# Performance work log

Measured on AMD Instinct MI355X. Metric: run time of the kernel, lower is better.

Reference implementation:

```python
import jax, jax.numpy as jnp
import numpy as np

NH = 8  # num_heads
EPS_LN = 1e-5
BN_DENOM = float(np.sqrt(1.0 + 1e-5))  # eval-mode BN with running_mean=0, running_var=1


def _layernorm(x, g, b):
    m = jnp.mean(x, axis=-1, keepdims=True)
    v = jnp.var(x, axis=-1, keepdims=True)
    return (x - m) * jax.lax.rsqrt(v + EPS_LN) * g + b


def _rope(q, k):
    # q,k: [B, H, T, D]
    t, d = q.shape[2], q.shape[3]
    half = d // 2
    pos = jnp.arange(t, dtype=q.dtype)[:, None]
    idx = jnp.arange(half, dtype=q.dtype)[None, :]
    inv_freq = 1.0 / (10000.0 ** (idx / half))
    ang = pos * inv_freq  # [T, half]
    sin = jnp.sin(ang)[None, None]
    cos = jnp.cos(ang)[None, None]

    def rot(x):
        x1, x2 = x[..., :half], x[..., half:]
        return jnp.concatenate([x1 * cos - x2 * sin, x1 * sin + x2 * cos], axis=-1)

    return rot(q), rot(k)


def _sep_conv(y, dw, pw):
    # y: [B, C, T]; dw: [C, 1, K]; pw: [O, C]
    c = y.shape[1]
    k = dw.shape[-1]
    y = jax.lax.conv_general_dilated(
        y, dw, window_strides=(2,), padding=[(k // 2, k // 2)],
        dimension_numbers=('NCH', 'OIH', 'NCH'), feature_group_count=c)
    return jnp.einsum('bct,oc->bot', y, pw)


def _attn(h, Wq, bq, Wk, bk, Wv, bv, Wo, bo):
    b, t, e = h.shape
    hd = e // NH
    scale = hd ** -0.5

    def split(z):
        return jnp.transpose(z.reshape(b, t, NH, hd), (0, 2, 1, 3))

    q = split(h @ Wq.T + bq)
    k = split(h @ Wk.T + bk)
    v = split(h @ Wv.T + bv)
    q, k = _rope(q, k)
    logits = jnp.einsum('bhtd,bhsd->bhts', q, k) * scale
    attn = jax.nn.softmax(logits, axis=-1)
    ctx = jnp.einsum('bhts,bhsd->bhtd', attn, v)
    ctx = jnp.transpose(ctx, (0, 2, 1, 3)).reshape(b, t, e)
    return ctx @ Wo.T + bo


def setup_inputs() -> dict:
    key = jax.random.key(0)
    ks = jax.random.split(key, 40)
    B, T, Cin = 8, 4096, 64
    E, L, MLP = 256, 6, 1024
    s = 0.02
    p = {}
    p['x'] = jax.random.normal(ks[0], (B, T, Cin), jnp.float32)
    p['conv1_dw'] = jax.random.normal(ks[1], (Cin, 1, 7), jnp.float32) * s
    p['conv1_pw'] = jax.random.normal(ks[2], (64, Cin), jnp.float32) * s
    p['bn1_g'] = jnp.ones((64,), jnp.float32)
    p['bn1_b'] = jnp.zeros((64,), jnp.float32)
    p['conv2_dw'] = jax.random.normal(ks[3], (64, 1, 7), jnp.float32) * s
    p['conv2_pw'] = jax.random.normal(ks[4], (128, 64), jnp.float32) * s
    p['bn2_g'] = jnp.ones((128,), jnp.float32)
    p['bn2_b'] = jnp.zeros((128,), jnp.float32)
    p['proj_w'] = jax.random.normal(ks[5], (E, 128), jnp.float32) * s
    p['proj_b'] = jnp.zeros((E,), jnp.float32)
    p['cls_tok'] = jax.random.normal(ks[6], (1, 1, E), jnp.float32) * s
    p['Wq'] = jax.random.normal(ks[7], (L, E, E), jnp.float32) * s
    p['bq'] = jnp.zeros((L, E), jnp.float32)
    p['Wk'] = jax.random.normal(ks[8], (L, E, E), jnp.float32) * s
    p['bk'] = jnp.zeros((L, E), jnp.float32)
    p['Wv'] = jax.random.normal(ks[9], (L, E, E), jnp.float32) * s
    p['bv'] = jnp.zeros((L, E), jnp.float32)
    p['Wo'] = jax.random.normal(ks[10], (L, E, E), jnp.float32) * s
    p['bo'] = jnp.zeros((L, E), jnp.float32)
    p['ln1_g'] = jnp.ones((L, E), jnp.float32)
    p['ln1_b'] = jnp.zeros((L, E), jnp.float32)
    p['mlp_w1'] = jax.random.normal(ks[11], (L, MLP, E), jnp.float32) * s
    p['mlp_b1'] = jnp.zeros((L, MLP), jnp.float32)
    p['mlp_w2'] = jax.random.normal(ks[12], (L, E, MLP), jnp.float32) * s
    p['mlp_b2'] = jnp.zeros((L, E), jnp.float32)
    p['ln2_g'] = jnp.ones((L, E), jnp.float32)
    p['ln2_b'] = jnp.zeros((L, E), jnp.float32)
    p['lat_w'] = jax.random.normal(ks[13], (E, E), jnp.float32) * s
    p['lat_b'] = jnp.zeros((E,), jnp.float32)
    p['latn_g'] = jnp.ones((E,), jnp.float32)
    p['latn_b'] = jnp.zeros((E,), jnp.float32)
    p['ts_w'] = jax.random.normal(ks[14], (1, E), jnp.float32) * s
    p['ts_b'] = jnp.zeros((1,), jnp.float32)
    return p


def reference(x, conv1_dw, conv1_pw, bn1_g, bn1_b, conv2_dw, conv2_pw, bn2_g, bn2_b,
              proj_w, proj_b, cls_tok, Wq, bq, Wk, bk, Wv, bv, Wo, bo,
              ln1_g, ln1_b, mlp_w1, mlp_b1, mlp_w2, mlp_b2, ln2_g, ln2_b,
              lat_w, lat_b, latn_g, latn_b, ts_w, ts_b):
    B = x.shape[0]
    y = jnp.transpose(x, (0, 2, 1))  # [B, C, T]
    y = _sep_conv(y, conv1_dw, conv1_pw)
    y = (y / BN_DENOM) * bn1_g[None, :, None] + bn1_b[None, :, None]
    y = jax.nn.gelu(y, approximate=False)
    y = _sep_conv(y, conv2_dw, conv2_pw)
    y = (y / BN_DENOM) * bn2_g[None, :, None] + bn2_b[None, :, None]
    y = jax.nn.gelu(y, approximate=False)
    y = jnp.transpose(y, (0, 2, 1))  # [B, T', 128]
    h = y @ proj_w.T + proj_b  # [B, T', E]
    h = jnp.concatenate([jnp.broadcast_to(cls_tok, (B, 1, h.shape[-1])), h], axis=1)
    L = Wq.shape[0]
    for i in range(L):
        a = _attn(h, Wq[i], bq[i], Wk[i], bk[i], Wv[i], bv[i], Wo[i], bo[i])
        h = _layernorm(h + a, ln1_g[i], ln1_b[i])
        m = jax.nn.gelu(h @ mlp_w1[i].T + mlp_b1[i], approximate=False) @ mlp_w2[i].T + mlp_b2[i]
        h = _layernorm(h + m, ln2_g[i], ln2_b[i])
    h = _layernorm(h @ lat_w.T + lat_b, latn_g, latn_b)
    logits = h[:, 1:] @ ts_w.T + ts_b  # per-time-step logits (CLS excluded)
    return logits
```

## Files before the change

### kernel.cpp

```cpp
#include <hip/hip_runtime.h>
#include <hip/hip_bf16.h>
#include <math.h>

typedef __hip_bfloat16 bf16;
typedef __attribute__((ext_vector_type(8))) short bf16x8_t;
typedef __attribute__((ext_vector_type(4))) short bf16x4_t;
typedef __attribute__((ext_vector_type(4))) float f32x4_t;

#define BN_RDENOM 0.9999950000374997f
#define EPS_LN 1e-5f
#define ATTN_SCALE 0.17677669529663687f
#define S_LEN 1025
#define S_PAD 1088
#define E_DIM 256
#define NHEAD 8
#define HDIM 32
#define MROWS (8 * S_LEN)
#define WSLOT 786432

__device__ __forceinline__ float bf(const bf16 v) { return __bfloat162float(v); }
__device__ __forceinline__ bf16 tobf(float v) { return __float2bfloat16(v); }
__device__ __forceinline__ short bfbits(float v) {
    bf16 t = __float2bfloat16(v); short s; __builtin_memcpy(&s, &t, 2); return s;
}
__device__ __forceinline__ float gelu_exact(float x) {
    return 0.5f * x * (1.0f + erff(x * 0.70710678118654752f));
}

#define DPP_ROR(x, N) __int_as_float(__builtin_amdgcn_update_dpp(0, __float_as_int(x), 0x120 + (N), 0xF, 0xF, false))
__device__ __forceinline__ float row_allsum(float x) {
    x = x + DPP_ROR(x, 1);
    x = x + DPP_ROR(x, 2);
    x = x + DPP_ROR(x, 4);
    x = x + DPP_ROR(x, 8);
    return x;
}

__global__ __launch_bounds__(256) void cvt_w(const float* __restrict__ src,
    bf16* __restrict__ dst, int n)
{
    int i = (blockIdx.x * 256 + threadIdx.x) * 4;
    if (i >= n) return;
    f32x4_t v = *(const f32x4_t*)(src + i);
    bf16x4_t o;
    #pragma unroll
    for (int j = 0; j < 4; ++j) o[j] = bfbits(v[j]);
    *(bf16x4_t*)((short*)dst + i) = o;
}

__global__ __launch_bounds__(256) void cvt_layer6(const float* __restrict__ wq,
    const float* __restrict__ wk, const float* __restrict__ wv, const float* __restrict__ wo,
    const float* __restrict__ w1, const float* __restrict__ w2, bf16* __restrict__ dst)
{
    int l = blockIdx.y;
    int i = (blockIdx.x * 256 + threadIdx.x) * 4;
    const float* s; int off;
    if (i < 262144) {
        s = (i < 65536) ? wq : (i < 131072) ? wk : (i < 196608) ? wv : wo;
        s += (size_t)l * 65536;
        off = i & 65535;
    } else if (i < 524288) { s = w1 + (size_t)l * 262144; off = i - 262144; }
    else                   { s = w2 + (size_t)l * 262144; off = i - 524288; }
    f32x4_t v = *(const f32x4_t*)(s + off);
    bf16x4_t o;
    #pragma unroll
    for (int j = 0; j < 4; ++j) o[j] = bfbits(v[j]);
    *(bf16x4_t*)((short*)dst + (size_t)l * WSLOT + i) = o;
}

__global__ __launch_bounds__(256) void conv_sep1(const float* __restrict__ x,
    const float* __restrict__ dw, const float* __restrict__ pw,
    const float* __restrict__ g, const float* __restrict__ bb,
    bf16* __restrict__ out)
{
    __shared__ float xs[70][64];
    __shared__ float dy[32][64];
    __shared__ float pws[64][65];
    __shared__ float dws[64][7];
    int blk = blockIdx.x;
    int tile = blk & 63, b = blk >> 6;
    int t0 = tile * 32;
    int tid = threadIdx.x;
    int tbase = t0 * 2 - 3;
    for (int i = tid; i < 70 * 64; i += 256) {
        int r = i >> 6, c = i & 63;
        int t = tbase + r;
        xs[r][c] = (t >= 0 && t < 4096) ? x[((size_t)b * 4096 + t) * 64 + c] : 0.f;
    }
    for (int i = tid; i < 64 * 7; i += 256) dws[i / 7][i % 7] = dw[i];
    for (int i = tid; i < 64 * 64; i += 256) pws[i >> 6][i & 63] = pw[i];
    __syncthreads();
    for (int i = tid; i < 32 * 64; i += 256) {
        int tl = i >> 6, c = i & 63;
        float s = 0.f;
        #pragma unroll
        for (int j = 0; j < 7; ++j) s += xs[2 * tl + j][c] * dws[c][j];
        dy[tl][c] = s;
    }
    __syncthreads();
    for (int i = tid; i < 32 * 64; i += 256) {
        int tl = i >> 6, o = i & 63;
        float s = 0.f;
        #pragma unroll 8
        for (int c = 0; c < 64; ++c) s += dy[tl][c] * pws[o][c];
        s = s * BN_RDENOM * g[o] + bb[o];
        out[((size_t)(b * 2048 + t0 + tl)) * 64 + o] = tobf(gelu_exact(s));
    }
}

__global__ __launch_bounds__(256) void conv_sep2(const bf16* __restrict__ x,
    const float* __restrict__ dw, const float* __restrict__ pw,
    const float* __restrict__ g, const float* __restrict__ bb,
    bf16* __restrict__ out)
{
    __shared__ float xs[70][64];
    __shared__ float dy[32][64];
    __shared__ float pws[128][65];
    __shared__ float dws[64][7];
    int blk = blockIdx.x;
    int tile = blk & 31, b = blk >> 5;
    int t0 = tile * 32;
    int tid = threadIdx.x;
    int tbase = t0 * 2 - 3;
    for (int i = tid; i < 70 * 64; i += 256) {
        int r = i >> 6, c = i & 63;
        int t = tbase + r;
        xs[r][c] = (t >= 0 && t < 2048) ? bf(x[((size_t)b * 2048 + t) * 64 + c]) : 0.f;
    }
    for (int i = tid; i < 64 * 7; i += 256) dws[i / 7][i % 7] = dw[i];
    for (int i = tid; i < 128 * 64; i += 256) pws[i >> 6][i & 63] = pw[i];
    __syncthreads();
    for (int i = tid; i < 32 * 64; i += 256) {
        int tl = i >> 6, c = i & 63;
        float s = 0.f;
        #pragma unroll
        for (int j = 0; j < 7; ++j) s += xs[2 * tl + j][c] * dws[c][j];
        dy[tl][c] = s;
    }
    __syncthreads();
    for (int i = tid; i < 32 * 128; i += 256) {
        int tl = i >> 7, o = i & 127;
        float s = 0.f;
        #pragma unroll 8
        for (int c = 0; c < 64; ++c) s += dy[tl][c] * pws[o][c];
        s = s * BN_RDENOM * g[o] + bb[o];
        out[((size_t)(b * 1024 + t0 + tl)) * 128 + o] = tobf(gelu_exact(s));
    }
}

template <int ACT>
__global__ __launch_bounds__(256) void gemm_bf(const bf16* __restrict__ A,
    const bf16* __restrict__ W, const float* __restrict__ bias,
    bf16* __restrict__ C, int M, int N, int K)
{
    __shared__ short As[64 * 72];
    __shared__ short Bs[64 * 72];
    int tid = threadIdx.x;
    int wave = tid >> 6, lane = tid & 63, quad = lane >> 4, l16 = lane & 15;
    int wm = wave & 1, wn = wave >> 1;
    int m0 = blockIdx.x * 64, n0 = blockIdx.y * 64;

    f32x4_t zero4 = {0.f, 0.f, 0.f, 0.f};
    f32x4_t acc[2][2];
    acc[0][0] = zero4; acc[0][1] = zero4; acc[1][0] = zero4; acc[1][1] = zero4;

    int srow = tid >> 2, skc = (tid & 3) * 16;
    for (int k0 = 0; k0 < K; k0 += 64) {
        {
            int m = m0 + srow;
            bf16x8_t a0 = {}, a1 = {};
            if (m < M) {
                a0 = *(const bf16x8_t*)(A + (size_t)m * K + k0 + skc);
                a1 = *(const bf16x8_t*)(A + (size_t)m * K + k0 + skc + 8);
            }
            *(bf16x8_t*)(&As[srow * 72 + skc])     = a0;
            *(bf16x8_t*)(&As[srow * 72 + skc + 8]) = a1;
        }
        {
            const bf16* wp = W + (size_t)(n0 + srow) * K + k0 + skc;
            *(bf16x8_t*)(&Bs[srow * 72 + skc])     = *(const bf16x8_t*)(wp);
            *(bf16x8_t*)(&Bs[srow * 72 + skc + 8]) = *(const bf16x8_t*)(wp + 8);
        }
        __syncthreads();
        #pragma unroll
        for (int ks = 0; ks < 2; ++ks) {
            bf16x8_t a[2], b[2];
            #pragma unroll
            for (int mi = 0; mi < 2; ++mi)
                a[mi] = *(bf16x8_t*)(&As[(wm * 32 + mi * 16 + l16) * 72 + ks * 32 + quad * 8]);
            #pragma unroll
            for (int ni = 0; ni < 2; ++ni)
                b[ni] = *(bf16x8_t*)(&Bs[(wn * 32 + ni * 16 + l16) * 72 + ks * 32 + quad * 8]);
            #pragma unroll
            for (int mi = 0; mi < 2; ++mi)
                #pragma unroll
                for (int ni = 0; ni < 2; ++ni)
                    acc[mi][ni] = __builtin_amdgcn_mfma_f32_16x16x32_bf16(a[mi], b[ni], acc[mi][ni], 0, 0, 0);
        }
        __syncthreads();
    }
    #pragma unroll
    for (int mi = 0; mi < 2; ++mi) {
        #pragma unroll
        for (int ni = 0; ni < 2; ++ni) {
            int col = n0 + wn * 32 + ni * 16 + l16;
            float bv = bias[col];
            #pragma unroll
            for (int r = 0; r < 4; ++r) {
                int row = m0 + wm * 32 + mi * 16 + quad * 4 + r;
                if (row < M) {
                    float v = acc[mi][ni][r] + bv;
                    if (ACT == 1) v = gelu_exact(v);
                    C[(size_t)row * N + col] = tobf(v);
                }
            }
        }
    }
}

template <int ACT>
__global__ __launch_bounds__(256) void gemm_bf128(const bf16* __restrict__ A,
    const bf16* __restrict__ W, const float* __restrict__ bias,
    bf16* __restrict__ C, int M, int N, int K)
{
    __shared__ short As[128 * 72];
    __shared__ short Bs[64 * 72];
    int tid = threadIdx.x;
    int wave = tid >> 6, lane = tid & 63, quad = lane >> 4, l16 = lane & 15;
    int wm = wave & 1, wn = wave >> 1;
    int m0 = blockIdx.x * 128, n0 = blockIdx.y * 64;

    f32x4_t zero4 = {0.f, 0.f, 0.f, 0.f};
    f32x4_t acc[4][2];
    #pragma unroll
    for (int i = 0; i < 4; ++i) { acc[i][0] = zero4; acc[i][1] = zero4; }

    int srow = tid >> 2, skc = (tid & 3) * 16;
    for (int k0 = 0; k0 < K; k0 += 64) {
        #pragma unroll
        for (int p = 0; p < 2; ++p) {
            int row = srow + p * 64;
            int m = m0 + row;
            bf16x8_t a0 = {}, a1 = {};
            if (m < M) {
                a0 = *(const bf16x8_t*)(A + (size_t)m * K + k0 + skc);
                a1 = *(const bf16x8_t*)(A + (size_t)m * K + k0 + skc + 8);
            }
            *(bf16x8_t*)(&As[row * 72 + skc])     = a0;
            *(bf16x8_t*)(&As[row * 72 + skc + 8]) = a1;
        }
        {
            const bf16* wp = W + (size_t)(n0 + srow) * K + k0 + skc;
            *(bf16x8_t*)(&Bs[srow * 72 + skc])     = *(const bf16x8_t*)(wp);
            *(bf16x8_t*)(&Bs[srow * 72 + skc + 8]) = *(const bf16x8_t*)(wp + 8);
        }
        __syncthreads();
        #pragma unroll
        for (int ks = 0; ks < 2; ++ks) {
            bf16x8_t a[4], b[2];
            #pragma unroll
            for (int mi = 0; mi < 4; ++mi)
                a[mi] = *(bf16x8_t*)(&As[(wm * 64 + mi * 16 + l16) * 72 + ks * 32 + quad * 8]);
            #pragma unroll
            for (int ni = 0; ni < 2; ++ni)
                b[ni] = *(bf16x8_t*)(&Bs[(wn * 32 + ni * 16 + l16) * 72 + ks * 32 + quad * 8]);
            #pragma unroll
            for (int mi = 0; mi < 4; ++mi)
                #pragma unroll
                for (int ni = 0; ni < 2; ++ni)
                    acc[mi][ni] = __builtin_amdgcn_mfma_f32_16x16x32_bf16(a[mi], b[ni], acc[mi][ni], 0, 0, 0);
        }
        __syncthreads();
    }
    #pragma unroll
    for (int mi = 0; mi < 4; ++mi) {
        #pragma unroll
        for (int ni = 0; ni < 2; ++ni) {
            int col = n0 + wn * 32 + ni * 16 + l16;
            float bv = bias[col];
            #pragma unroll
            for (int r = 0; r < 4; ++r) {
                int row = m0 + wm * 64 + mi * 16 + quad * 4 + r;
                if (row < M) {
                    float v = acc[mi][ni][r] + bv;
                    if (ACT == 1) v = gelu_exact(v);
                    C[(size_t)row * N + col] = tobf(v);
                }
            }
        }
    }
}

__global__ __launch_bounds__(256) void gemm_qkv128(const bf16* __restrict__ A,
    const bf16* __restrict__ Wqkv, const float* __restrict__ bq,
    const float* __restrict__ bk, const float* __restrict__ bv,
    bf16* __restrict__ qo, bf16* __restrict__ ko, bf16* __restrict__ vo, int M)
{
    const int K = 256, N = 256;
    __shared__ short As[128 * 72];
    __shared__ short Bs[64 * 72];
    int part = blockIdx.y >> 2;
    int n0 = (blockIdx.y & 3) * 64;
    const bf16* W     = Wqkv + (size_t)part * 65536;
    const float* bias = (part == 0) ? bq : (part == 1) ? bk : bv;
    bf16* C           = (part == 0) ? qo : (part == 1) ? ko : vo;
    bool dorope = (part < 2);
    float oscale = (part == 0) ? ATTN_SCALE : 1.0f;

    int tid = threadIdx.x;
    int wave = tid >> 6, lane = tid & 63, quad = lane >> 4, l16 = lane & 15;
    int wm = wave & 1, wn = wave >> 1;
    int m0 = blockIdx.x * 128;

    f32x4_t zero4 = {0.f, 0.f, 0.f, 0.f};
    f32x4_t acc[4][2];
    #pragma unroll
    for (int i = 0; i < 4; ++i) { acc[i][0] = zero4; acc[i][1] = zero4; }

    int srow = tid >> 2, skc = (tid & 3) * 16;
    for (int k0 = 0; k0 < K; k0 += 64) {
        #pragma unroll
        for (int p = 0; p < 2; ++p) {
            int row = srow + p * 64;
            int m = m0 + row;
            bf16x8_t a0 = {}, a1 = {};
            if (m < M) {
                a0 = *(const bf16x8_t*)(A + (size_t)m * K + k0 + skc);
                a1 = *(const bf16x8_t*)(A + (size_t)m * K + k0 + skc + 8);
            }
            *(bf16x8_t*)(&As[row * 72 + skc])     = a0;
            *(bf16x8_t*)(&As[row * 72 + skc + 8]) = a1;
        }
        {
            const bf16* wp = W + (size_t)(n0 + srow) * K + k0 + skc;
            *(bf16x8_t*)(&Bs[srow * 72 + skc])     = *(const bf16x8_t*)(wp);
            *(bf16x8_t*)(&Bs[srow * 72 + skc + 8]) = *(const bf16x8_t*)(wp + 8);
        }
        __syncthreads();
        #pragma unroll
        for (int ks = 0; ks < 2; ++ks) {
            bf16x8_t a[4], b[2];
            #pragma unroll
            for (int mi = 0; mi < 4; ++mi)
                a[mi] = *(bf16x8_t*)(&As[(wm * 64 + mi * 16 + l16) * 72 + ks * 32 + quad * 8]);
            #pragma unroll
            for (int ni = 0; ni < 2; ++ni)
                b[ni] = *(bf16x8_t*)(&Bs[(wn * 32 + ni * 16 + l16) * 72 + ks * 32 + quad * 8]);
            #pragma unroll
            for (int mi = 0; mi < 4; ++mi)
                #pragma unroll
                for (int ni = 0; ni < 2; ++ni)
                    acc[mi][ni] = __builtin_amdgcn_mfma_f32_16x16x32_bf16(a[mi], b[ni], acc[mi][ni], 0, 0, 0);
        }
        __syncthreads();
    }
    int col0 = n0 + wn * 32 + l16;
    float b1v = bias[col0], b2v = bias[col0 + 16];
    float invf = powf(10000.f, -(float)l16 * (1.f / 16.f));
    #pragma unroll
    for (int mi = 0; mi < 4; ++mi) {
        #pragma unroll
        for (int r = 0; r < 4; ++r) {
            int row = m0 + wm * 64 + mi * 16 + quad * 4 + r;
            if (row >= M) continue;
            int bb = row / S_LEN, t = row - bb * S_LEN;
            float x1 = acc[mi][0][r] + b1v;
            float x2 = acc[mi][1][r] + b2v;
            if (dorope) {
                float ang = (float)t * invf;
                float sn, cs;
                __sincosf(ang, &sn, &cs);
                float y1 = (x1 * cs - x2 * sn) * oscale;
                float y2 = (x1 * sn + x2 * cs) * oscale;
                x1 = y1; x2 = y2;
            }
            size_t obase = ((size_t)bb * S_PAD + t) * N;
            C[obase + col0]      = tobf(x1);
            C[obase + col0 + 16] = tobf(x2);
        }
    }
}

__global__ __launch_bounds__(256) void assemble_h(const bf16* __restrict__ tmp,
    const float* __restrict__ cls, bf16* __restrict__ h)
{
    int row = blockIdx.x;
    int tid = threadIdx.x;
    int b = row / S_LEN, t = row % S_LEN;
    bf16 v = (t == 0) ? tobf(cls[tid]) : tmp[((size_t)(b * 1024 + t - 1)) * E_DIM + tid];
    h[(size_t)row * E_DIM + tid] = v;
}

__global__ __launch_bounds__(256) void attn_mfma(const bf16* __restrict__ Q,
    const bf16* __restrict__ K, const bf16* __restrict__ V, bf16* __restrict__ O)
{
    __shared__ short VTs[2][32 * 72];
    __shared__ short Ps[4][16 * 72];
    int blk = blockIdx.x;
    int bh = blk & 63;
    int qt = blk >> 6;
    int hh = bh & 7, b = bh >> 3;
    int tid = threadIdx.x;
    int wave = tid >> 6, lane = tid & 63, quad = lane >> 4, l16 = lane & 15;
    int q0 = qt * 64 + wave * 16;
    const size_t bSp = (size_t)b * S_PAD;
    const size_t bS  = (size_t)b * S_LEN;
    const size_t hoff = (size_t)hh * HDIM;
    const bf16* Qb = Q + bSp * E_DIM + hoff;
    const bf16* Kb = K + bSp * E_DIM + hoff;
    const bf16* Vb = V + bSp * E_DIM + hoff;

    f32x4_t zero4 = {0.f, 0.f, 0.f, 0.f};
    bf16x8_t qfrag = *(const bf16x8_t*)(Qb + (size_t)(q0 + l16) * E_DIM + quad * 8);
    f32x4_t o0 = zero4, o1 = zero4;
    float lsum[4] = {0.f, 0.f, 0.f, 0.f};

    int vs = tid >> 2, vd = (tid & 3) * 8;
    short* myP = Ps[wave];

    bf16x8_t vpre = *(const bf16x8_t*)(Vb + (size_t)vs * E_DIM + vd);

    for (int c = 0; c < 17; ++c) {
        int s0 = c * 64;
        short* VT = VTs[c & 1];
        #pragma unroll
        for (int j = 0; j < 8; ++j) VT[(vd + j) * 72 + vs] = vpre[j];
        if (c < 16)
            vpre = *(const bf16x8_t*)(Vb + (size_t)(s0 + 64 + vs) * E_DIM + vd);
        f32x4_t sc[4];
        #pragma unroll
        for (int kk = 0; kk < 4; ++kk) {
            bf16x8_t kf = *(const bf16x8_t*)(Kb + (size_t)(s0 + kk * 16 + l16) * E_DIM + quad * 8);
            sc[kk] = __builtin_amdgcn_mfma_f32_16x16x32_bf16(qfrag, kf, zero4, 0, 0, 0);
        }
        #pragma unroll
        for (int r = 0; r < 4; ++r) {
            float ps = 0.f;
            #pragma unroll
            for (int kk = 0; kk < 4; ++kk) {
                int s = s0 + kk * 16 + l16;
                float raw = (s < S_LEN) ? sc[kk][r] : -1e30f;
                float p = __expf(raw);
                ps += p;
                myP[(quad * 4 + r) * 72 + kk * 16 + l16] = bfbits(p);
            }
            lsum[r] += ps;
        }
        __syncthreads();
        #pragma unroll
        for (int half = 0; half < 2; ++half) {
            int off = half * 32 + quad * 8;
            bf16x8_t pf  = *(bf16x8_t*)(&myP[l16 * 72 + off]);
            bf16x8_t vf0 = *(bf16x8_t*)(&VT[l16 * 72 + off]);
            bf16x8_t vf1 = *(bf16x8_t*)(&VT[(16 + l16) * 72 + off]);
            o0 = __builtin_amdgcn_mfma_f32_16x16x32_bf16(pf, vf0, o0, 0, 0, 0);
            o1 = __builtin_amdgcn_mfma_f32_16x16x32_bf16(pf, vf1, o1, 0, 0, 0);
        }
    }
    #pragma unroll
    for (int r = 0; r < 4; ++r) {
        int qrow = q0 + quad * 4 + r;
        if (qrow < S_LEN) {
            float rs = 1.f / row_allsum(lsum[r]);
            O[(bS + qrow) * E_DIM + hoff + l16]      = tobf(o0[r] * rs);
            O[(bS + qrow) * E_DIM + hoff + 16 + l16] = tobf(o1[r] * rs);
        }
    }
}

__global__ __launch_bounds__(256) void ln_kernel(const bf16* __restrict__ X,
    const bf16* __restrict__ R, const float* __restrict__ g,
    const float* __restrict__ b, bf16* __restrict__ out)
{
    int wave = threadIdx.x >> 6, lane = threadIdx.x & 63;
    int row0 = blockIdx.x * 8 + wave * 2;
    size_t base0 = (size_t)row0 * E_DIM + lane * 4;
    size_t base1 = base0 + E_DIM;
    float v0[4], v1[4];
    {
        bf16x4_t xa = *(const bf16x4_t*)(X + base0);
        bf16x4_t xb = *(const bf16x4_t*)(X + base1);
        #pragma unroll
        for (int i = 0; i < 4; ++i) {
            bf16 t; short s;
            s = xa[i]; __builtin_memcpy(&t, &s, 2); v0[i] = bf(t);
            s = xb[i]; __builtin_memcpy(&t, &s, 2); v1[i] = bf(t);
        }
    }
    if (R) {
        bf16x4_t ra = *(const bf16x4_t*)(R + base0);
        bf16x4_t rb = *(const bf16x4_t*)(R + base1);
        #pragma unroll
        for (int i = 0; i < 4; ++i) {
            bf16 t; short s;
            s = ra[i]; __builtin_memcpy(&t, &s, 2); v0[i] += bf(t);
            s = rb[i]; __builtin_memcpy(&t, &s, 2); v1[i] += bf(t);
        }
    }
    float s0 = v0[0] + v0[1] + v0[2] + v0[3];
    float s1 = v1[0] + v1[1] + v1[2] + v1[3];
    #pragma unroll
    for (int off = 32; off; off >>= 1) { s0 += __shfl_xor(s0, off); s1 += __shfl_xor(s1, off); }
    float m0 = s0 * (1.f / 256.f), m1 = s1 * (1.f / 256.f);
    float w0 = 0.f, w1 = 0.f;
    #pragma unroll
    for (int i = 0; i < 4; ++i) {
        v0[i] -= m0; w0 += v0[i] * v0[i];
        v1[i] -= m1; w1 += v1[i] * v1[i];
    }
    #pragma unroll
    for (int off = 32; off; off >>= 1) { w0 += __shfl_xor(w0, off); w1 += __shfl_xor(w1, off); }
    float r0 = rsqrtf(w0 * (1.f / 256.f) + EPS_LN);
    float r1 = rsqrtf(w1 * (1.f / 256.f) + EPS_LN);
    int c = lane * 4;
    bf16x4_t oa, ob;
    #pragma unroll
    for (int i = 0; i < 4; ++i) {
        oa[i] = bfbits(v0[i] * r0 * g[c + i] + b[c + i]);
        ob[i] = bfbits(v1[i] * r1 * g[c + i] + b[c + i]);
    }
    *(bf16x4_t*)(out + base0) = oa;
    *(bf16x4_t*)(out + base1) = ob;
}

__global__ __launch_bounds__(256) void ts_kernel(const bf16* __restrict__ H,
    const float* __restrict__ w, const float* __restrict__ tb,
    float* __restrict__ out)
{
    int wid = (blockIdx.x << 2) + (threadIdx.x >> 6);
    int lane = threadIdx.x & 63;
    int b = wid >> 10, t = wid & 1023;
    const bf16* row = H + ((size_t)(b * S_LEN + t + 1)) * E_DIM;
    float acc = 0.f;
    for (int e = lane; e < E_DIM; e += 64) acc += bf(row[e]) * w[e];
    #pragma unroll
    for (int off = 32; off; off >>= 1) acc += __shfl_down(acc, off, 64);
    if (lane == 0) out[wid] = acc + tb[0];
}

extern "C" void kernel_launch(void* const* d_in, const int* in_sizes, int n_in,
                              void* d_out, int out_size, void* d_ws, size_t ws_size,
                              hipStream_t stream)
{
    (void)in_sizes; (void)n_in; (void)out_size; (void)ws_size;
    const float* X        = (const float*)d_in[0];
    const float* CONV1_DW = (const float*)d_in[1];
    const float* CONV1_PW = (const float*)d_in[2];
    const float* BN1_G    = (const float*)d_in[3];
    const float* BN1_B    = (const float*)d_in[4];
    const float* CONV2_DW = (const float*)d_in[5];
    const float* CONV2_PW = (const float*)d_in[6];
    const float* BN2_G    = (const float*)d_in[7];
    const float* BN2_B    = (const float*)d_in[8];
    const float* PROJ_W   = (const float*)d_in[9];
    const float* PROJ_B   = (const float*)d_in[10];
    const float* CLS      = (const float*)d_in[11];
    const float* WQ       = (const float*)d_in[12];
    const float* BQ       = (const float*)d_in[13];
    const float* WK       = (const float*)d_in[14];
    const float* BK       = (const float*)d_in[15];
    const float* WV       = (const float*)d_in[16];
    const float* BV       = (const float*)d_in[17];
    const float* WO       = (const float*)d_in[18];
    const float* BO       = (const float*)d_in[19];
    const float* LN1G     = (const float*)d_in[20];
    const float* LN1B     = (const float*)d_in[21];
    const float* W1       = (const float*)d_in[22];
    const float* B1       = (const float*)d_in[23];
    const float* W2       = (const float*)d_in[24];
    const float* B2       = (const float*)d_in[25];
    const float* LN2G     = (const float*)d_in[26];
    const float* LN2B     = (const float*)d_in[27];
    const float* LATW     = (const float*)d_in[28];
    const float* LATB     = (const float*)d_in[29];
    const float* LATNG    = (const float*)d_in[30];
    const float* LATNB    = (const float*)d_in[31];
    const float* TSW      = (const float*)d_in[32];
    const float* TSB      = (const float*)d_in[33];

    const size_t SROW  = (size_t)MROWS * E_DIM;
    const size_t SPROW = (size_t)8 * S_PAD * E_DIM;
    bf16* h    = (bf16*)d_ws;
    bf16* bufB = h + SROW;
    bf16* r0   = bufB + SROW;
    bf16* q  = r0;
    bf16* k  = r0 + SPROW;
    bf16* v  = r0 + 2 * SPROW;
    bf16* cx = r0 + 3 * SPROW;
    bf16* wall = cx + SROW;
    bf16* pslot = wall + 6 * WSLOT;
    bf16* y1 = r0;
    bf16* y2 = r0 + SROW;
    bf16* mid = r0;

    conv_sep1<<<dim3(512), dim3(256), 0, stream>>>(X, CONV1_DW, CONV1_PW, BN1_G, BN1_B, y1);
    conv_sep2<<<dim3(256), dim3(256), 0, stream>>>(y1, CONV2_DW, CONV2_PW, BN2_G, BN2_B, y2);
    cvt_w<<<dim3(32), dim3(256), 0, stream>>>(PROJ_W, pslot, 32768);
    gemm_bf<0><<<dim3(128, 4), dim3(256), 0, stream>>>(y2, pslot, PROJ_B, bufB, 8192, 256, 128);
    assemble_h<<<dim3(MROWS), dim3(256), 0, stream>>>(bufB, CLS, h);
    cvt_layer6<<<dim3(768, 6), dim3(256), 0, stream>>>(WQ, WK, WV, WO, W1, W2, wall);

    for (int l = 0; l < 6; ++l) {
        bf16* wslot = wall + (size_t)l * WSLOT;
        gemm_qkv128<<<dim3(65, 12), dim3(256), 0, stream>>>(h, wslot,
            BQ + l * 256, BK + l * 256, BV + l * 256, q, k, v, MROWS);
        attn_mfma<<<dim3(64 * 17), dim3(256), 0, stream>>>(q, k, v, cx);
        gemm_bf<0><<<dim3(129, 4), dim3(256), 0, stream>>>(cx, wslot + 196608, BO + l * 256, bufB, MROWS, 256, 256);
        ln_kernel<<<dim3(MROWS / 8), dim3(256), 0, stream>>>(h, bufB, LN1G + l * 256, LN1B + l * 256, h);
        gemm_bf128<1><<<dim3(65, 16), dim3(256), 0, stream>>>(h, wslot + 262144, B1 + l * 1024, mid, MROWS, 1024, 256);
        gemm_bf<0><<<dim3(129, 4), dim3(256), 0, stream>>>(mid, wslot + 524288, B2 + l * 256, bufB, MROWS, 256, 1024);
        ln_kernel<<<dim3(MROWS / 8), dim3(256), 0, stream>>>(h, bufB, LN2G + l * 256, LN2B + l * 256, h);
    }

    cvt_w<<<dim3(64), dim3(256), 0, stream>>>(LATW, pslot, 65536);
    gemm_bf<0><<<dim3(129, 4), dim3(256), 0, stream>>>(h, pslot, LATB, bufB, MROWS, 256, 256);
    ln_kernel<<<dim3(MROWS / 8), dim3(256), 0, stream>>>(bufB, nullptr, LATNG, LATNB, r0);
    ts_kernel<<<dim3(2048), dim3(256), 0, stream>>>(r0, TSW, TSB, (float*)d_out);
}
```

Before: 839.0 us.

## Write V transposed from QKV GEMM and read it directly in attention

```diff
diff --git a/kernel.cpp b/kernel.cpp
--- a/kernel.cpp
+++ b/kernel.cpp
@@ -303,8 +303,6 @@
     int n0 = (blockIdx.y & 3) * 64;
     const bf16* W     = Wqkv + (size_t)part * 65536;
     const float* bias = (part == 0) ? bq : (part == 1) ? bk : bv;
-    bf16* C           = (part == 0) ? qo : (part == 1) ? ko : vo;
-    bool dorope = (part < 2);
     float oscale = (part == 0) ? ATTN_SCALE : 1.0f;
 
     int tid = threadIdx.x;
@@ -356,28 +354,53 @@
     }
     int col0 = n0 + wn * 32 + l16;
     float b1v = bias[col0], b2v = bias[col0 + 16];
-    float invf = powf(10000.f, -(float)l16 * (1.f / 16.f));
-    #pragma unroll
-    for (int mi = 0; mi < 4; ++mi) {
-        #pragma unroll
-        for (int r = 0; r < 4; ++r) {
-            int row = m0 + wm * 64 + mi * 16 + quad * 4 + r;
-            if (row >= M) continue;
-            int bb = row / S_LEN, t = row - bb * S_LEN;
-            float x1 = acc[mi][0][r] + b1v;
-            float x2 = acc[mi][1][r] + b2v;
-            if (dorope) {
+    if (part == 2) {
+        int hA = (n0 >> 5) + wn;
+        #pragma unroll
+        for (int mi = 0; mi < 4; ++mi) {
+            #pragma unroll
+            for (int r = 0; r < 4; ++r) {
+                int row = m0 + wm * 64 + mi * 16 + quad * 4 + r;
+                if (row >= M) continue;
+                int bb = row / S_LEN, t = row - bb * S_LEN;
+                size_t rbase = ((size_t)(bb * NHEAD + hA)) * HDIM;
+                vo[(rbase + l16) * S_PAD + t]      = tobf(acc[mi][0][r] + b1v);
+                vo[(rbase + l16 + 16) * S_PAD + t] = tobf(acc[mi][1][r] + b2v);
+            }
+        }
+    } else {
+        bf16* C = (part == 0) ? qo : ko;
+        float invf = powf(10000.f, -(float)l16 * (1.f / 16.f));
+        #pragma unroll
+        for (int mi = 0; mi < 4; ++mi) {
+            #pragma unroll
+            for (int r = 0; r < 4; ++r) {
+                int row = m0 + wm * 64 + mi * 16 + quad * 4 + r;
+                if (row >= M) continue;
+                int bb = row / S_LEN, t = row - bb * S_LEN;
+                float x1 = acc[mi][0][r] + b1v;
+                float x2 = acc[mi][1][r] + b2v;
                 float ang = (float)t * invf;
                 float sn, cs;
                 __sincosf(ang, &sn, &cs);
                 float y1 = (x1 * cs - x2 * sn) * oscale;
                 float y2 = (x1 * sn + x2 * cs) * oscale;
-                x1 = y1; x2 = y2;
-            }
-            size_t obase = ((size_t)bb * S_PAD + t) * N;
-            C[obase + col0]      = tobf(x1);
-            C[obase + col0 + 16] = tobf(x2);
-        }
+                size_t obase = ((size_t)bb * S_PAD + t) * N;
+                C[obase + col0]      = tobf(y1);
+                C[obase + col0 + 16] = tobf(y2);
+            }
+        }
+    }
+}
+
+__global__ __launch_bounds__(256) void zero_vpad(bf16* __restrict__ vt)
+{
+    int bh = blockIdx.x;
+    bf16* base = vt + (size_t)bh * HDIM * S_PAD;
+    const int PADW = S_PAD - S_LEN;
+    for (int i = threadIdx.x; i < HDIM * PADW; i += 256) {
+        int d = i / PADW, s = i - d * PADW;
+        base[(size_t)d * S_PAD + S_LEN + s] = tobf(0.f);
     }
 }
 
@@ -392,9 +415,8 @@
 }
 
 __global__ __launch_bounds__(256) void attn_mfma(const bf16* __restrict__ Q,
-    const bf16* __restrict__ K, const bf16* __restrict__ V, bf16* __restrict__ O)
-{
-    __shared__ short VTs[2][32 * 72];
+    const bf16* __restrict__ K, const bf16* __restrict__ VT, bf16* __restrict__ O)
+{
     __shared__ short Ps[4][16 * 72];
     int blk = blockIdx.x;
     int bh = blk & 63;
@@ -408,25 +430,18 @@
     const size_t hoff = (size_t)hh * HDIM;
     const bf16* Qb = Q + bSp * E_DIM + hoff;
     const bf16* Kb = K + bSp * E_DIM + hoff;
-    const bf16* Vb = V + bSp * E_DIM + hoff;
+    const bf16* VTb = VT + (size_t)(b * NHEAD + hh) * HDIM * S_PAD;
 
     f32x4_t zero4 = {0.f, 0.f, 0.f, 0.f};
     bf16x8_t qfrag = *(const bf16x8_t*)(Qb + (size_t)(q0 + l16) * E_DIM + quad * 8);
     f32x4_t o0 = zero4, o1 = zero4;
     float lsum[4] = {0.f, 0.f, 0.f, 0.f};
-
-    int vs = tid >> 2, vd = (tid & 3) * 8;
     short* myP = Ps[wave];
-
-    bf16x8_t vpre = *(const bf16x8_t*)(Vb + (size_t)vs * E_DIM + vd);
+    const bf16* v0p = VTb + (size_t)l16 * S_PAD;
+    const bf16* v1p = VTb + (size_t)(l16 + 16) * S_PAD;
 
     for (int c = 0; c < 17; ++c) {
         int s0 = c * 64;
-        short* VT = VTs[c & 1];
-        #pragma unroll
-        for (int j = 0; j < 8; ++j) VT[(vd + j) * 72 + vs] = vpre[j];
-        if (c < 16)
-            vpre = *(const bf16x8_t*)(Vb + (size_t)(s0 + 64 + vs) * E_DIM + vd);
         f32x4_t sc[4];
         #pragma unroll
         for (int kk = 0; kk < 4; ++kk) {
@@ -446,13 +461,13 @@
             }
             lsum[r] += ps;
         }
-        __syncthreads();
+        asm volatile("s_waitcnt lgkmcnt(0)" ::: "memory");
         #pragma unroll
         for (int half = 0; half < 2; ++half) {
             int off = half * 32 + quad * 8;
             bf16x8_t pf  = *(bf16x8_t*)(&myP[l16 * 72 + off]);
-            bf16x8_t vf0 = *(bf16x8_t*)(&VT[l16 * 72 + off]);
-            bf16x8_t vf1 = *(bf16x8_t*)(&VT[(16 + l16) * 72 + off]);
+            bf16x8_t vf0 = *(const bf16x8_t*)(v0p + s0 + off);
+            bf16x8_t vf1 = *(const bf16x8_t*)(v1p + s0 + off);
             o0 = __builtin_amdgcn_mfma_f32_16x16x32_bf16(pf, vf0, o0, 0, 0, 0);
             o1 = __builtin_amdgcn_mfma_f32_16x16x32_bf16(pf, vf1, o1, 0, 0, 0);
         }
@@ -599,6 +614,7 @@
     gemm_bf<0><<<dim3(128, 4), dim3(256), 0, stream>>>(y2, pslot, PROJ_B, bufB, 8192, 256, 128);
     assemble_h<<<dim3(MROWS), dim3(256), 0, stream>>>(bufB, CLS, h);
     cvt_layer6<<<dim3(768, 6), dim3(256), 0, stream>>>(WQ, WK, WV, WO, W1, W2, wall);
+    zero_vpad<<<dim3(64), dim3(256), 0, stream>>>(v);
 
     for (int l = 0; l < 6; ++l) {
         bf16* wslot = wall + (size_t)l * WSLOT;
```

New measurement: 1.064 ms. +26.8%, slower.
